# Kernel tuning notes

Measured on AMD Instinct MI355X. Metric: run time of the kernel, lower is better.

Reference implementation:

```python
import jax, jax.numpy as jnp
import numpy as np

B, C_IN, H, W = 16, 256, 64, 64
D, K = 128, 1024  # embed_dim, nb_entries


def setup_inputs() -> dict:
    key = jax.random.key(0)
    k1, k2, k3, k4 = jax.random.split(key, 4)
    x = jax.random.normal(k1, (B, C_IN, H, W), dtype=jnp.float32)
    conv_w = jax.random.normal(k2, (C_IN, D), dtype=jnp.float32) * 0.05
    conv_b = jax.random.normal(k3, (D,), dtype=jnp.float32) * 0.05
    embed = jax.random.normal(k4, (D, K), dtype=jnp.float32)
    return {"x": x, "conv_w": conv_w, "conv_b": conv_b, "embed": embed}


def reference(x, conv_w, conv_b, embed):
    # 1x1 conv == per-pixel matmul; go straight to NHWC layout.
    z = jnp.einsum('bchw,cd->bhwd', x, conv_w) + conv_b        # [B,H,W,D]
    flat = z.reshape(-1, D)                                     # [N,D]
    # Squared-euclidean distances to codebook columns (||f||^2 - 2 f.E + ||e||^2).
    dist = (jnp.sum(flat * flat, axis=1, keepdims=True)
            - 2.0 * (flat @ embed)
            + jnp.sum(embed * embed, axis=0, keepdims=True))    # [N,K]
    embed_ind = jnp.argmin(dist, axis=1)                        # [N] int
    embed_ind = embed_ind.reshape(B, H, W)
    quantize = jnp.take(embed.T, embed_ind, axis=0)             # [B,H,W,D] gather
    diff = jnp.mean((jax.lax.stop_gradient(quantize) - z) ** 2)
    quantize = z + jax.lax.stop_gradient(quantize - z)          # straight-through
    return quantize.transpose(0, 3, 1, 2), diff, embed_ind
```

## Files before the change

### kernel.cpp

```cpp
#include <hip/hip_runtime.h>

typedef __attribute__((ext_vector_type(4))) float f32x4;
typedef __attribute__((ext_vector_type(8))) short bf16x8;

constexpr int CIN = 256;
constexpr int D   = 128;
constexpr int K   = 1024;
constexpr int HW  = 4096;
constexpr int MT  = 128;
constexpr int DIFF_OFF = 8388608;
constexpr int IDX_OFF  = 8388609;

__device__ float g_scratch[16 + K];
__device__ __align__(16) uint4 g_efrags[64 * 8 * 64];
__device__ __align__(16) uint4 g_wfrags[8 * 8 * 3 * 64];
__device__ __align__(16) float g_embedT[K * D];

__device__ inline unsigned short f2bf(float f) {
    unsigned u = __float_as_uint(f);
    u = u + 0x7fff + ((u >> 16) & 1);
    return (unsigned short)(u >> 16);
}
__device__ inline float bf2f(unsigned short h) {
    return __uint_as_float(((unsigned)h) << 16);
}
__device__ inline void split3(float v, short& a, short& b, short& c) {
    unsigned short h = f2bf(v); float r1 = v - bf2f(h);
    unsigned short m = f2bf(r1); float r2 = r1 - bf2f(m);
    a = (short)h; b = (short)m; c = (short)f2bf(r2);
}

__device__ inline void gload_lds16(const uint4* g, uint4* l) {
    __builtin_amdgcn_global_load_lds(
        (const __attribute__((address_space(1))) unsigned int*)g,
        (__attribute__((address_space(3))) unsigned int*)l,
        16, 0, 0);
}

__global__ void vq_init(const float* __restrict__ embed) {
    int k = blockIdx.x * 256 + threadIdx.x;
    if (k == 0) g_scratch[0] = 0.0f;
    if (k < K) {
        float s = 0.0f;
        for (int d = 0; d < D; ++d) { float v = embed[d * K + k]; s += v * v; }
        g_scratch[16 + k] = s;
    }
}

__global__ void vq_prep2(const float* __restrict__ embed) {
    __shared__ float tile[32][33];
    int kb = blockIdx.x >> 2, db = blockIdx.x & 3;
    int t = threadIdx.x, tk = t & 31, td = t >> 5;
    #pragma unroll
    for (int dd = 0; dd < 4; ++dd)
        tile[td * 4 + dd][tk] = embed[(size_t)(db * 32 + td * 4 + dd) * K + kb * 32 + tk];
    __syncthreads();
    #pragma unroll
    for (int dd = 0; dd < 4; ++dd)
        g_embedT[(size_t)(kb * 32 + td * 4 + dd) * D + db * 32 + tk] = tile[tk][td * 4 + dd];
}

__global__ void vq_prep(const float* __restrict__ embed) {
    int kt = blockIdx.x >> 2, dc = blockIdx.x & 3;
    int l  = threadIdx.x;
    int k  = kt * 16 + (l & 15);
    int d0 = dc * 32 + (l >> 4) * 8;
    unsigned short hi[8], lo[8];
    #pragma unroll
    for (int j = 0; j < 8; ++j) {
        float v = embed[(size_t)(d0 + j) * K + k];
        hi[j] = f2bf(v);
        lo[j] = f2bf(v - bf2f(hi[j]));
    }
    uint4 H, L;
    H.x = (unsigned)hi[0] | ((unsigned)hi[1] << 16);
    H.y = (unsigned)hi[2] | ((unsigned)hi[3] << 16);
    H.z = (unsigned)hi[4] | ((unsigned)hi[5] << 16);
    H.w = (unsigned)hi[6] | ((unsigned)hi[7] << 16);
    L.x = (unsigned)lo[0] | ((unsigned)lo[1] << 16);
    L.y = (unsigned)lo[2] | ((unsigned)lo[3] << 16);
    L.z = (unsigned)lo[4] | ((unsigned)lo[5] << 16);
    L.w = (unsigned)lo[6] | ((unsigned)lo[7] << 16);
    g_efrags[(kt * 8 + dc * 2 + 0) * 64 + l] = H;
    g_efrags[(kt * 8 + dc * 2 + 1) * 64 + l] = L;
}

__global__ void vq_prepw(const float* __restrict__ conv_w) {
    int cb = blockIdx.x >> 3, db = blockIdx.x & 7, l = threadIdx.x;
    int c0 = cb * 32 + (l >> 4) * 8, d = db * 16 + (l & 15);
    short s1[8], s2[8], s3[8];
    #pragma unroll
    for (int j = 0; j < 8; ++j)
        split3(conv_w[(size_t)(c0 + j) * D + d], s1[j], s2[j], s3[j]);
    #pragma unroll
    for (int s = 0; s < 3; ++s) {
        const short* sp = s == 0 ? s1 : s == 1 ? s2 : s3;
        uint4 P;
        P.x = (unsigned)(unsigned short)sp[0] | ((unsigned)(unsigned short)sp[1] << 16);
        P.y = (unsigned)(unsigned short)sp[2] | ((unsigned)(unsigned short)sp[3] << 16);
        P.z = (unsigned)(unsigned short)sp[4] | ((unsigned)(unsigned short)sp[5] << 16);
        P.w = (unsigned)(unsigned short)sp[6] | ((unsigned)(unsigned short)sp[7] << 16);
        g_wfrags[((cb * 8 + db) * 3 + s) * 64 + l] = P;
    }
}

#define MFMA(a, bb, c) __builtin_amdgcn_mfma_f32_16x16x32_bf16(a, bb, c, 0, 0, 0)

__global__ __launch_bounds__(256, 2) void vq_main(
    const float* __restrict__ x, const float* __restrict__ conv_b,
    float* __restrict__ out)
{
    __shared__ __align__(16) uint4 ebuf[4096];
    __shared__ float e2_s[K];
    __shared__ float tbuf[4 * 16 * 36];
    __shared__ int   ks_s[MT];
    __shared__ float red_s[4];

    const int t    = threadIdx.x;
    const int lane = t & 63;
    const int w    = t >> 6;
    const int wg   = blockIdx.x;
    const int n0   = wg * MT;
    const int b    = n0 >> 12;
    const int hw0  = n0 & 4095;
    const int pxb  = w * 32;
    const int lp   = lane & 15;
    const int lg   = lane >> 4;

    for (int k = t; k < K; k += 256) e2_s[k] = g_scratch[16 + k];

    f32x4 Cz[2][8];
    #pragma unroll
    for (int db = 0; db < 8; ++db) {
        float bv = conv_b[db * 16 + lp];
        Cz[0][db] = (f32x4){bv, bv, bv, bv};
        Cz[1][db] = Cz[0][db];
    }
    {
        #pragma unroll
        for (int i = 0; i < 6; ++i)
            gload_lds16(&g_wfrags[(w * 6 + i) * 64 + lane], &ebuf[(w * 6 + i) * 64]);
        asm volatile("s_waitcnt vmcnt(0)" ::: "memory");
        __syncthreads();

        const float* xl = x + (size_t)b * CIN * HW + (size_t)(lg * 8) * HW
                          + hw0 + pxb + lp;
        for (int cb = 0; cb < 8; ++cb) {
            float v[2][8];
            #pragma unroll
            for (int rb = 0; rb < 2; ++rb)
                #pragma unroll
                for (int j = 0; j < 8; ++j)
                    v[rb][j] = xl[(size_t)(cb * 32 + j) * HW + rb * 16];
            if (cb < 7) {
                const uint4* wsrc = g_wfrags + (size_t)(cb + 1) * 1536;
                uint4* wdst = ebuf + ((cb + 1) & 1) * 1536;
                #pragma unroll
                for (int i = 0; i < 6; ++i)
                    gload_lds16(&wsrc[(w * 6 + i) * 64 + lane], &wdst[(w * 6 + i) * 64]);
            }
            bf16x8 X1[2], X2[2], X3[2];
            #pragma unroll
            for (int rb = 0; rb < 2; ++rb)
                #pragma unroll
                for (int j = 0; j < 8; ++j) {
                    short a, bb, c;
                    split3(v[rb][j], a, bb, c);
                    X1[rb][j] = a; X2[rb][j] = bb; X3[rb][j] = c;
                }
            const uint4* wb = ebuf + (cb & 1) * 1536;
            #pragma unroll
            for (int db = 0; db < 8; ++db) {
                bf16x8 W1 = *(const bf16x8*)&wb[(db * 3 + 0) * 64 + lane];
                bf16x8 W2 = *(const bf16x8*)&wb[(db * 3 + 1) * 64 + lane];
                bf16x8 W3 = *(const bf16x8*)&wb[(db * 3 + 2) * 64 + lane];
                Cz[0][db] = MFMA(X1[0], W1, Cz[0][db]);
                Cz[1][db] = MFMA(X1[1], W1, Cz[1][db]);
                Cz[0][db] = MFMA(X1[0], W2, Cz[0][db]);
                Cz[1][db] = MFMA(X1[1], W2, Cz[1][db]);
                Cz[0][db] = MFMA(X2[0], W1, Cz[0][db]);
                Cz[1][db] = MFMA(X2[1], W1, Cz[1][db]);
                Cz[0][db] = MFMA(X1[0], W3, Cz[0][db]);
                Cz[1][db] = MFMA(X1[1], W3, Cz[1][db]);
                Cz[0][db] = MFMA(X2[0], W2, Cz[0][db]);
                Cz[1][db] = MFMA(X2[1], W2, Cz[1][db]);
                Cz[0][db] = MFMA(X3[0], W1, Cz[0][db]);
                Cz[1][db] = MFMA(X3[1], W1, Cz[1][db]);
            }
            asm volatile("s_waitcnt vmcnt(0)" ::: "memory");
            __syncthreads();
        }
    }

    bf16x8 A2h[2][4], A2l[2][4];
    {
        float* tb = tbuf + w * 576;
        #pragma unroll
        for (int rb = 0; rb < 2; ++rb) {
            #pragma unroll
            for (int dc = 0; dc < 4; ++dc) {
                #pragma unroll
                for (int h = 0; h < 2; ++h)
                    #pragma unroll
                    for (int r = 0; r < 4; ++r)
                        tb[(lg * 4 + r) * 36 + h * 16 + lp] = Cz[rb][dc * 2 + h][r];
                asm volatile("s_waitcnt lgkmcnt(0)" ::: "memory");
                f32x4 a0 = *(const f32x4*)&tb[lp * 36 + lg * 8];
                f32x4 a1 = *(const f32x4*)&tb[lp * 36 + lg * 8 + 4];
                #pragma unroll
                for (int j = 0; j < 8; ++j) {
                    float zv = -2.0f * (j < 4 ? a0[j] : a1[j - 4]);
                    unsigned short hb = f2bf(zv);
                    A2h[rb][dc][j] = (short)hb;
                    A2l[rb][dc][j] = (short)f2bf(zv - bf2f(hb));
                }
                asm volatile("s_waitcnt lgkmcnt(0)" ::: "memory");
            }
        }
    }

    const uint4* gfr = g_efrags;
    {
        #pragma unroll
        for (int i = 0; i < 8; ++i)
            gload_lds16(&gfr[(w * 8 + i) * 64 + lane], &ebuf[(w * 8 + i) * 64]);
        asm volatile("s_waitcnt vmcnt(0)" ::: "memory");
        __syncthreads();
    }

    float v1[8], v2[8]; int i1[8], i2[8];
    #pragma unroll
    for (int q = 0; q < 8; ++q) { v1[q] = 3.4e38f; v2[q] = 3.4e38f; i1[q] = 0; i2[q] = 0; }

    for (int c = 0; c < 16; ++c) {
        if (c < 15) {
            const uint4* esrc = gfr + (size_t)(c + 1) * 2048;
            uint4* edst = ebuf + ((c + 1) & 1) * 2048;
            #pragma unroll
            for (int i = 0; i < 8; ++i)
                gload_lds16(&esrc[(w * 8 + i) * 64 + lane], &edst[(w * 8 + i) * 64]);
        }
        const bf16x8* eb = (const bf16x8*)&ebuf[(c & 1) * 2048];
        #pragma unroll
        for (int ktl = 0; ktl < 4; ++ktl) {
            int kt = c * 4 + ktl;
            bf16x8 Bh[4], Bl[4];
            #pragma unroll
            for (int dc = 0; dc < 4; ++dc) {
                Bh[dc] = eb[(ktl * 8 + dc * 2 + 0) * 64 + lane];
                Bl[dc] = eb[(ktl * 8 + dc * 2 + 1) * 64 + lane];
            }
            float e2v = e2_s[kt * 16 + lp];
            f32x4 C0 = (f32x4){e2v, e2v, e2v, e2v};
            f32x4 C1 = C0;
            __builtin_amdgcn_s_setprio(1);
            #pragma unroll
            for (int dc = 0; dc < 4; ++dc) {
                C0 = MFMA(A2h[0][dc], Bh[dc], C0);
                C1 = MFMA(A2h[1][dc], Bh[dc], C1);
                C0 = MFMA(A2l[0][dc], Bh[dc], C0);
                C1 = MFMA(A2l[1][dc], Bh[dc], C1);
                C0 = MFMA(A2h[0][dc], Bl[dc], C0);
                C1 = MFMA(A2h[1][dc], Bl[dc], C1);
            }
            __builtin_amdgcn_s_setprio(0);
            int kk = kt * 16 + lp;
            #pragma unroll
            for (int rb = 0; rb < 2; ++rb) {
                f32x4 C = rb ? C1 : C0;
                #pragma unroll
                for (int r = 0; r < 4; ++r) {
                    int q = rb * 4 + r;
                    float s = C[r];
                    bool lt1 = s < v1[q], lt2 = s < v2[q];
                    v2[q] = lt1 ? v1[q] : (lt2 ? s  : v2[q]);
                    i2[q] = lt1 ? i1[q] : (lt2 ? kk : i2[q]);
                    v1[q] = lt1 ? s  : v1[q];
                    i1[q] = lt1 ? kk : i1[q];
                }
            }
        }
        if (c < 15) asm volatile("s_waitcnt vmcnt(0)" ::: "memory");
        __syncthreads();
    }

    #pragma unroll
    for (int off = 1; off < 16; off <<= 1) {
        #pragma unroll
        for (int q = 0; q < 8; ++q) {
            float b1 = __shfl_xor(v1[q], off); int bi1 = __shfl_xor(i1[q], off);
            float b2 = __shfl_xor(v2[q], off); int bi2 = __shfl_xor(i2[q], off);
            bool bf = (b1 < v1[q]) || (b1 == v1[q] && bi1 < i1[q]);
            float cv = bf ? v1[q] : b1;  int ci = bf ? i1[q] : bi1;
            float wv = bf ? b2 : v2[q];  int wi = bf ? bi2 : i2[q];
            v1[q] = bf ? b1 : v1[q];     i1[q] = bf ? bi1 : i1[q];
            bool c2 = (cv < wv) || (cv == wv && ci < wi);
            v2[q] = c2 ? cv : wv;        i2[q] = c2 ? ci : wi;
        }
    }

    float dacc = 0.0f;
    #pragma unroll
    for (int q = 0; q < 8; ++q) {
        const int rb = q >> 2, r = q & 3;
        const int k1 = i1[q], k2 = i2[q];
        float s1 = 0.0f, s2 = 0.0f;
        #pragma unroll
        for (int db = 0; db < 8; ++db) {
            float zv = Cz[rb][db][r];
            s1 += zv * g_embedT[(size_t)k1 * D + db * 16 + lp];
            s2 += zv * g_embedT[(size_t)k2 * D + db * 16 + lp];
        }
        #pragma unroll
        for (int off = 1; off < 16; off <<= 1) {
            s1 += __shfl_xor(s1, off);
            s2 += __shfl_xor(s2, off);
        }
        float d1 = e2_s[k1] - 2.0f * s1;
        float d2 = e2_s[k2] - 2.0f * s2;
        bool p2 = (d2 < d1) || (d2 == d1 && k2 < k1);
        int ks = p2 ? k2 : k1;
        #pragma unroll
        for (int db = 0; db < 8; ++db) {
            float zv = Cz[rb][db][r];
            float qv = g_embedT[(size_t)ks * D + db * 16 + lp];
            float df = qv - zv;
            dacc += df * df;
        }
        if (lp == 0) {
            int px = pxb + rb * 16 + lg * 4 + r;
            ks_s[px] = ks;
            out[IDX_OFF + n0 + px] = (float)ks;
        }
    }
    #pragma unroll
    for (int off = 1; off <= 32; off <<= 1) dacc += __shfl_xor(dacc, off);
    if (lane == 0) red_s[w] = dacc;
    __syncthreads();

    {
        int px = t & 127, half = t >> 7;
        int ks = ks_s[px];
        const f32x4* ep = (const f32x4*)&g_embedT[(size_t)ks * D + half * 64];
        float* ob = out + (size_t)b * D * HW + hw0 + px;
        #pragma unroll
        for (int d4 = 0; d4 < 16; ++d4) {
            f32x4 q4 = ep[d4];
            int d = half * 64 + d4 * 4;
            #pragma unroll
            for (int cc = 0; cc < 4; ++cc)
                ob[(size_t)(d + cc) * HW] = q4[cc];
        }
    }
    if (t == 0) atomicAdd(&g_scratch[0], red_s[0] + red_s[1] + red_s[2] + red_s[3]);
}

__global__ void vq_final(float* __restrict__ out) {
    out[DIFF_OFF] = g_scratch[0] / 8388608.0f;
}

extern "C" void kernel_launch(void* const* d_in, const int* in_sizes, int n_in,
                              void* d_out, int out_size, void* d_ws, size_t ws_size,
                              hipStream_t stream) {
    const float* x      = (const float*)d_in[0];
    const float* conv_w = (const float*)d_in[1];
    const float* conv_b = (const float*)d_in[2];
    const float* embed  = (const float*)d_in[3];
    float* out = (float*)d_out;

    vq_init  <<<4,   256, 0, stream>>>(embed);
    vq_prep2 <<<128, 256, 0, stream>>>(embed);
    vq_prep  <<<256, 64,  0, stream>>>(embed);
    vq_prepw <<<64,  64,  0, stream>>>(conv_w);
    vq_main  <<<512, 256, 0, stream>>>(x, conv_b, out);
    vq_final <<<1,   1,   0, stream>>>(out);
}
```

Baseline: 102.2 us.

## Merge prep kernels, truncate-split activations, stagger per-wave LDS access order

```diff
diff --git a/kernel.cpp b/kernel.cpp
--- a/kernel.cpp
+++ b/kernel.cpp
@@ -29,6 +29,14 @@
     unsigned short m = f2bf(r1); float r2 = r1 - bf2f(m);
     a = (short)h; b = (short)m; c = (short)f2bf(r2);
 }
+__device__ inline void split3t(float v, short& a, short& b, short& c) {
+    unsigned u1 = __float_as_uint(v) & 0xffff0000u;
+    float r1 = v - __uint_as_float(u1);
+    unsigned u2 = __float_as_uint(r1) & 0xffff0000u;
+    float r2 = r1 - __uint_as_float(u2);
+    a = (short)(u1 >> 16); b = (short)(u2 >> 16);
+    c = (short)(__float_as_uint(r2) >> 16);
+}
 
 __device__ inline void gload_lds16(const uint4* g, uint4* l) {
     __builtin_amdgcn_global_load_lds(
@@ -37,70 +45,69 @@
         16, 0, 0);
 }
 
-__global__ void vq_init(const float* __restrict__ embed) {
-    int k = blockIdx.x * 256 + threadIdx.x;
-    if (k == 0) g_scratch[0] = 0.0f;
-    if (k < K) {
+__global__ void vq_prep_all(const float* __restrict__ embed,
+                            const float* __restrict__ conv_w) {
+    const int bi = blockIdx.x;
+    const int t  = threadIdx.x;
+    if (bi < 128) {
+        __shared__ float tile[32][33];
+        int kb = bi >> 2, db = bi & 3;
+        int tk = t & 31, td = t >> 5;
+        #pragma unroll
+        for (int dd = 0; dd < 4; ++dd)
+            tile[td * 4 + dd][tk] =
+                embed[(size_t)(db * 32 + td * 4 + dd) * K + kb * 32 + tk];
+        __syncthreads();
+        #pragma unroll
+        for (int dd = 0; dd < 4; ++dd)
+            g_embedT[(size_t)(kb * 32 + td * 4 + dd) * D + db * 32 + tk] =
+                tile[tk][td * 4 + dd];
+    } else if (bi < 192) {
+        int kt = bi - 128, dc = t >> 6, l = t & 63;
+        int k  = kt * 16 + (l & 15);
+        int d0 = dc * 32 + (l >> 4) * 8;
+        unsigned short hi[8], lo[8];
+        #pragma unroll
+        for (int j = 0; j < 8; ++j) {
+            float v = embed[(size_t)(d0 + j) * K + k];
+            hi[j] = f2bf(v);
+            lo[j] = f2bf(v - bf2f(hi[j]));
+        }
+        uint4 H, L;
+        H.x = (unsigned)hi[0] | ((unsigned)hi[1] << 16);
+        H.y = (unsigned)hi[2] | ((unsigned)hi[3] << 16);
+        H.z = (unsigned)hi[4] | ((unsigned)hi[5] << 16);
+        H.w = (unsigned)hi[6] | ((unsigned)hi[7] << 16);
+        L.x = (unsigned)lo[0] | ((unsigned)lo[1] << 16);
+        L.y = (unsigned)lo[2] | ((unsigned)lo[3] << 16);
+        L.z = (unsigned)lo[4] | ((unsigned)lo[5] << 16);
+        L.w = (unsigned)lo[6] | ((unsigned)lo[7] << 16);
+        g_efrags[(kt * 8 + dc * 2 + 0) * 64 + l] = H;
+        g_efrags[(kt * 8 + dc * 2 + 1) * 64 + l] = L;
+    } else if (bi < 208) {
+        int old = (bi - 192) * 4 + (t >> 6), l = t & 63;
+        int cb = old >> 3, db = old & 7;
+        int c0 = cb * 32 + (l >> 4) * 8, d = db * 16 + (l & 15);
+        short s1[8], s2[8], s3[8];
+        #pragma unroll
+        for (int j = 0; j < 8; ++j)
+            split3(conv_w[(size_t)(c0 + j) * D + d], s1[j], s2[j], s3[j]);
+        #pragma unroll
+        for (int s = 0; s < 3; ++s) {
+            const short* sp = s == 0 ? s1 : s == 1 ? s2 : s3;
+            uint4 P;
+            P.x = (unsigned)(unsigned short)sp[0] | ((unsigned)(unsigned short)sp[1] << 16);
+            P.y = (unsigned)(unsigned short)sp[2] | ((unsigned)(unsigned short)sp[3] << 16);
+            P.z = (unsigned)(unsigned short)sp[4] | ((unsigned)(unsigned short)sp[5] << 16);
+            P.w = (unsigned)(unsigned short)sp[6] | ((unsigned)(unsigned short)sp[7] << 16);
+            g_wfrags[((cb * 8 + db) * 3 + s) * 64 + l] = P;
+        }
+    } else {
+        int k = (bi - 208) * 256 + t;
+        if (k == 0) g_scratch[0] = 0.0f;
         float s = 0.0f;
         for (int d = 0; d < D; ++d) { float v = embed[d * K + k]; s += v * v; }
         g_scratch[16 + k] = s;
-    }
-}
-
-__global__ void vq_prep2(const float* __restrict__ embed) {
-    __shared__ float tile[32][33];
-    int kb = blockIdx.x >> 2, db = blockIdx.x & 3;
-    int t = threadIdx.x, tk = t & 31, td = t >> 5;
-    #pragma unroll
-    for (int dd = 0; dd < 4; ++dd)
-        tile[td * 4 + dd][tk] = embed[(size_t)(db * 32 + td * 4 + dd) * K + kb * 32 + tk];
-    __syncthreads();
-    #pragma unroll
-    for (int dd = 0; dd < 4; ++dd)
-        g_embedT[(size_t)(kb * 32 + td * 4 + dd) * D + db * 32 + tk] = tile[tk][td * 4 + dd];
-}
-
-__global__ void vq_prep(const float* __restrict__ embed) {
-    int kt = blockIdx.x >> 2, dc = blockIdx.x & 3;
-    int l  = threadIdx.x;
-    int k  = kt * 16 + (l & 15);
-    int d0 = dc * 32 + (l >> 4) * 8;
-    unsigned short hi[8], lo[8];
-    #pragma unroll
-    for (int j = 0; j < 8; ++j) {
-        float v = embed[(size_t)(d0 + j) * K + k];
-        hi[j] = f2bf(v);
-        lo[j] = f2bf(v - bf2f(hi[j]));
-    }
-    uint4 H, L;
-    H.x = (unsigned)hi[0] | ((unsigned)hi[1] << 16);
-    H.y = (unsigned)hi[2] | ((unsigned)hi[3] << 16);
-    H.z = (unsigned)hi[4] | ((unsigned)hi[5] << 16);
-    H.w = (unsigned)hi[6] | ((unsigned)hi[7] << 16);
-    L.x = (unsigned)lo[0] | ((unsigned)lo[1] << 16);
-    L.y = (unsigned)lo[2] | ((unsigned)lo[3] << 16);
-    L.z = (unsigned)lo[4] | ((unsigned)lo[5] << 16);
-    L.w = (unsigned)lo[6] | ((unsigned)lo[7] << 16);
-    g_efrags[(kt * 8 + dc * 2 + 0) * 64 + l] = H;
-    g_efrags[(kt * 8 + dc * 2 + 1) * 64 + l] = L;
-}
-
-__global__ void vq_prepw(const float* __restrict__ conv_w) {
-    int cb = blockIdx.x >> 3, db = blockIdx.x & 7, l = threadIdx.x;
-    int c0 = cb * 32 + (l >> 4) * 8, d = db * 16 + (l & 15);
-    short s1[8], s2[8], s3[8];
-    #pragma unroll
-    for (int j = 0; j < 8; ++j)
-        split3(conv_w[(size_t)(c0 + j) * D + d], s1[j], s2[j], s3[j]);
-    #pragma unroll
-    for (int s = 0; s < 3; ++s) {
-        const short* sp = s == 0 ? s1 : s == 1 ? s2 : s3;
-        uint4 P;
-        P.x = (unsigned)(unsigned short)sp[0] | ((unsigned)(unsigned short)sp[1] << 16);
-        P.y = (unsigned)(unsigned short)sp[2] | ((unsigned)(unsigned short)sp[3] << 16);
-        P.z = (unsigned)(unsigned short)sp[4] | ((unsigned)(unsigned short)sp[5] << 16);
-        P.w = (unsigned)(unsigned short)sp[6] | ((unsigned)(unsigned short)sp[7] << 16);
-        g_wfrags[((cb * 8 + db) * 3 + s) * 64 + l] = P;
     }
 }
 
@@ -165,12 +172,13 @@
                 #pragma unroll
                 for (int j = 0; j < 8; ++j) {
                     short a, bb, c;
-                    split3(v[rb][j], a, bb, c);
+                    split3t(v[rb][j], a, bb, c);
                     X1[rb][j] = a; X2[rb][j] = bb; X3[rb][j] = c;
                 }
             const uint4* wb = ebuf + (cb & 1) * 1536;
             #pragma unroll
-            for (int db = 0; db < 8; ++db) {
+            for (int dbi = 0; dbi < 8; ++dbi) {
+                int db = (dbi + 2 * w) & 7;
                 bf16x8 W1 = *(const bf16x8*)&wb[(db * 3 + 0) * 64 + lane];
                 bf16x8 W2 = *(const bf16x8*)&wb[(db * 3 + 1) * 64 + lane];
                 bf16x8 W3 = *(const bf16x8*)&wb[(db * 3 + 2) * 64 + lane];
@@ -242,7 +250,8 @@
         }
         const bf16x8* eb = (const bf16x8*)&ebuf[(c & 1) * 2048];
         #pragma unroll
-        for (int ktl = 0; ktl < 4; ++ktl) {
+        for (int ktli = 0; ktli < 4; ++ktli) {
+            int ktl = (ktli + w) & 3;
             int kt = c * 4 + ktl;
             bf16x8 Bh[4], Bl[4];
             #pragma unroll
@@ -368,10 +377,7 @@
     const float* embed  = (const float*)d_in[3];
     float* out = (float*)d_out;
 
-    vq_init  <<<4,   256, 0, stream>>>(embed);
-    vq_prep2 <<<128, 256, 0, stream>>>(embed);
-    vq_prep  <<<256, 64,  0, stream>>>(embed);
-    vq_prepw <<<64,  64,  0, stream>>>(conv_w);
-    vq_main  <<<512, 256, 0, stream>>>(x, conv_b, out);
-    vq_final <<<1,   1,   0, stream>>>(out);
-}
+    vq_prep_all<<<212, 256, 0, stream>>>(embed, conv_w);
+    vq_main    <<<512, 256, 0, stream>>>(x, conv_b, out);
+    vq_final   <<<1,   1,   0, stream>>>(out);
+}
```

Measured after the change: 161.2 us. 1.58x slower.
